# Optimization experiments

Measured on AMD Instinct MI355X. Metric: run time of the kernel, lower is better.

## Reference

```python
import jax, jax.numpy as jnp
import numpy as np

K = 5  # kernel_size per dim (dim=2 -> 25 kernels), B-spline degree 1, open spline


def spline_conv(x, edge_index, pseudo, W, root, bias):
    # x: [N, Cin], pseudo: [E, 2] in [0,1], W: [K*K, Cin, Cout]
    N = x.shape[0]
    src, dst = edge_index[0], edge_index[1]
    # Transform node features with every kernel weight once: [N, K*K, Cout]
    xk = jnp.einsum('ni,kio->nko', x, W)
    # Degree-1 open B-spline basis: v = u*(K-1); frac/1-frac weights over 2 knots per dim
    v = pseudo * (K - 1)
    bot = jnp.floor(v)
    frac = v - bot
    bot = bot.astype(jnp.int32)
    msg = jnp.zeros((src.shape[0], W.shape[2]), dtype=x.dtype)
    for s0 in (0, 1):
        for s1 in (0, 1):
            b0 = frac[:, 0] if s0 else (1.0 - frac[:, 0])
            b1 = frac[:, 1] if s1 else (1.0 - frac[:, 1])
            basis = b0 * b1  # [E]
            idx = (jnp.clip(bot[:, 0] + s0, 0, K - 1)
                   + K * jnp.clip(bot[:, 1] + s1, 0, K - 1))  # [E]
            msg = msg + basis[:, None] * xk[src, idx]  # gather [E, Cout]
    # scatter-max aggregation into target nodes; empty nodes -> 0 (PyG convention)
    agg = jax.ops.segment_max(msg, dst, num_segments=N)
    agg = jnp.where(jnp.isfinite(agg), agg, jnp.zeros_like(agg))
    return agg + x @ root + bias


def setup_inputs() -> dict:
    key = jax.random.key(0)
    ks = jax.random.split(key, 8)
    N, E, C = 50000, 1600000, 64
    Cin = C
    s = 1.0 / np.sqrt(25 * Cin)
    return {
        'x': jax.random.normal(ks[0], (N, C), dtype=jnp.float32),
        'edge_index': jax.random.randint(ks[1], (2, E), 0, N, dtype=jnp.int32),
        'edge_attr': jax.random.uniform(ks[2], (E, 2), dtype=jnp.float32),
        'W1': jax.random.normal(ks[3], (25, C, C), dtype=jnp.float32) * s,
        'root1': jax.random.normal(ks[4], (C, C), dtype=jnp.float32) / np.sqrt(C),
        'bias1': jnp.zeros((C,), dtype=jnp.float32),
        'W2': jax.random.normal(ks[5], (25, C, C), dtype=jnp.float32) * s,
        'root2': jax.random.normal(ks[6], (C, C), dtype=jnp.float32) / np.sqrt(C),
        'bias2': jnp.zeros((C,), dtype=jnp.float32),
    }


def reference(x, edge_index, edge_attr, W1, root1, bias1, W2, root2, bias2):
    h = jax.nn.relu(spline_conv(x, edge_index, edge_attr, W1, root1, bias1))
    out = spline_conv(h, edge_index, edge_attr, W2, root2, bias2)
    return out
```

## Files before the change

kernel.cpp:

```cpp
#include <hip/hip_runtime.h>
#include <hip/hip_bf16.h>
#include <math.h>

#define CHANNELS 64
#define KK 25
#define NBLK 26
#define NCOL (NBLK * CHANNELS)
#define NTILES (NCOL / 16)
#define ROWP 2560
#define CELL_BYTES 8192

#define BK_SHIFT 7
#define BK_W 128
#define BK_CAP 5120
#define BK_MAXNB 512
#define EDGES_PER_BLK 4096

typedef __attribute__((ext_vector_type(8))) short bf16x8;
typedef __attribute__((ext_vector_type(4))) float f32x4;
typedef __attribute__((ext_vector_type(2))) float f32x2;
typedef unsigned int u32;

__device__ __forceinline__ u32 f2bfu(float f) {
    u32 u = __float_as_uint(f);
    return (u + 0x7FFFu + ((u >> 16) & 1u)) >> 16;
}
__device__ __forceinline__ short f2bf(float f) { return (short)f2bfu(f); }

__device__ __forceinline__ void async_copy16(const void* g, void* l) {
    __builtin_amdgcn_global_load_lds(
        (const __attribute__((address_space(1))) u32*)g,
        (__attribute__((address_space(3))) u32*)l, 16, 0, 0);
}

template<int N> struct IC { static constexpr int v = N; };
template<int G, int GEND, class F>
__device__ __forceinline__ void unrollg(F f) {
    if constexpr (G < GEND) { f(IC<G>{}); unrollg<G + 1, GEND>(f); }
}

__device__ constexpr int cell_stores(int c) {
    return (c < KK) ? (((c % 5) != 0) ? 4 : 0) : 4;
}


__global__ __launch_bounds__(256) void prep_w(const float* __restrict__ W,
                                              const float* __restrict__ root,
                                              __hip_bfloat16* __restrict__ Wb) {
    int idx = blockIdx.x * 256 + threadIdx.x;
    if (idx >= NTILES * 2 * 64 * 8) return;
    int j = idx & 7;
    int l = (idx >> 3) & 63;
    int q = (idx >> 9) & 1;
    int t = idx >> 10;
    int cell = t >> 2;
    int o    = 4 * (l & 15) + (t & 3);
    int k    = q * 32 + (l >> 4) * 8 + j;
    float src = (cell < KK) ? W[cell * 4096 + k * 64 + o] : root[k * 64 + o];
    ((unsigned short*)Wb)[idx] = (unsigned short)f2bf(src);
}

__device__ __forceinline__ uint2 mkrec(int src, float v0f, float v1f) {
    const float v0 = v0f * 4.0f, v1 = v1f * 4.0f;
    const int p0 = max(min((int)floorf(v0), 3), 0);
    const int p1 = max(min((int)floorf(v1), 3), 0);
    const float f0 = v0 - (float)p0;
    const float f1 = v1 - (float)p1;
    const u32 f0q = min((u32)(f0 * 65536.0f), 65535u);
    const u32 f1q = min((u32)(f1 * 65536.0f), 65535u);
    uint2 rec;
    rec.x = (u32)src | ((u32)p0 << 16) | ((u32)p1 << 19);
    rec.y = f0q | (f1q << 16);
    return rec;
}


__global__ __launch_bounds__(256) void bucket_scatter(
    const int* __restrict__ ei, const float* __restrict__ ps,
    u32* __restrict__ bcur, uint2* __restrict__ bucketed, int E, int NB)
{
    __shared__ u32 lhist[BK_MAXNB];
    __shared__ u32 lbase[BK_MAXNB];
    const int t = threadIdx.x;
    const int e0 = blockIdx.x * EDGES_PER_BLK;
    for (int k = t; k < NB; k += 256) lhist[k] = 0;
    __syncthreads();
    u32 pk[16];
#pragma unroll
    for (int r = 0; r < 16; ++r) {
        const int e = e0 + r * 256 + t;
        u32 v = 0u;
        if (e < E) {
            const int bkt = ei[E + e] >> BK_SHIFT;
            const u32 lr = atomicAdd(&lhist[bkt], 1u);
            v = ((u32)bkt << 13) | lr;
        }
        pk[r] = v;
    }
    __syncthreads();
    for (int k = t; k < NB; k += 256) {
        const u32 h = lhist[k];
        lbase[k] = h ? atomicAdd(&bcur[k], h) : 0u;
    }
    __syncthreads();
#pragma unroll
    for (int r = 0; r < 16; ++r) {
        const int e = e0 + r * 256 + t;
        if (e < E) {
            const u32 v = pk[r];
            const int bkt = (int)(v >> 13);
            const u32 lr = v & 0x1FFFu;
            u32 slot = lbase[bkt] + lr;
            if (slot >= BK_CAP) slot = BK_CAP - 1;
            const int src = ei[e];
            const int dst = ei[E + e];
            uint2 rec = mkrec(src, ps[2 * e], ps[2 * e + 1]);
            rec.x |= (u32)(dst & (BK_W - 1)) << 22;
            bucketed[(size_t)bkt * BK_CAP + slot] = rec;
        }
    }
}

__global__ __launch_bounds__(256) void bucket_bases(
    const u32* __restrict__ bcur, u32* __restrict__ bbase, int NB)
{
    __shared__ u32 tmp[BK_MAXNB];
    const int t = threadIdx.x;
    for (int k = t; k < NB; k += 256) tmp[k] = min(bcur[k], (u32)BK_CAP);
    __syncthreads();
    if (t == 0) {
        u32 run = 0;
        for (int k = 0; k < NB; ++k) { const u32 c = tmp[k]; tmp[k] = run; run += c; }
    }
    __syncthreads();
    for (int k = t; k < NB; k += 256) bbase[k] = tmp[k];
}

__global__ __launch_bounds__(256) void bucket_sort(
    const uint2* __restrict__ bucketed, const u32* __restrict__ bcur,
    const u32* __restrict__ bbase, uint2* __restrict__ sorted,
    u32* __restrict__ cursor, int N)
{
    __shared__ __align__(16) uint2 buf[BK_CAP];
    __shared__ u32 lhist[BK_W + 1];
    __shared__ u32 lbase[BK_W + 1];
    const int b = blockIdx.x;
    const int t = threadIdx.x;
    const int cnt = (int)min(bcur[b], (u32)BK_CAP);
    const u32 gb = bbase[b];
    const uint2* __restrict__ in = bucketed + (size_t)b * BK_CAP;

    for (int k = t; k <= BK_W; k += 256) lhist[k] = 0;
    __syncthreads();
    for (int i = t; i < cnt; i += 256) {
        const u32 nl = (in[i].x >> 22) & (BK_W - 1);
        atomicAdd(&lhist[nl], 1u);
    }
    __syncthreads();
    if (t == 0) {
        u32 run = 0;
        for (int k = 0; k <= BK_W; ++k) { const u32 c = lhist[k]; lhist[k] = run; run += c; }
    }
    __syncthreads();
    for (int k = t; k <= BK_W; k += 256) lbase[k] = lhist[k];
    __syncthreads();
    for (int i = t; i < cnt; i += 256) {
        const uint2 r = in[i];
        const u32 nl = (r.x >> 22) & (BK_W - 1);
        const u32 p = atomicAdd(&lhist[nl], 1u);
        buf[p] = r;
    }
    __syncthreads();
    for (int i = t; i < cnt; i += 256) sorted[gb + i] = buf[i];
    for (int k = t; k <= BK_W; k += 256) {
        const int node = b * BK_W + k;
        if (node <= N) cursor[node] = gb + lbase[k];
    }
}

__global__ __launch_bounds__(256) void gemm_nb(
    const float* __restrict__ X, const __hip_bfloat16* __restrict__ Wb,
    char* __restrict__ XK, float* __restrict__ rootf, int N)
{
    __shared__ __align__(16) char lds[4][2][CELL_BYTES];
    const int lane = threadIdx.x & 63;
    const int wv   = threadIdx.x >> 6;
    const int rb   = blockIdx.x * 64 + wv * 16;
    const int m    = lane & 15;
    const int quad = lane >> 4;
    const int Nm1  = N - 1;

    const int rowc = min(rb + m, Nm1);
    const float* __restrict__ xp = X + (size_t)rowc * CHANNELS + quad * 8;
    float af[16];
    *(float4*)(af)      = *(const float4*)(xp);
    *(float4*)(af + 4)  = *(const float4*)(xp + 4);
    *(float4*)(af + 8)  = *(const float4*)(xp + 32);
    *(float4*)(af + 12) = *(const float4*)(xp + 36);
    bf16x8 A0, A1;
#pragma unroll
    for (int j = 0; j < 8; ++j) { A0[j] = f2bf(af[j]); A1[j] = f2bf(af[8 + j]); }

    const int r0 = rb + quad * 4;
    const char* __restrict__ wbc = (const char*)Wb;
    char* const ldsw = &lds[wv][0][0];

    auto stage = [&](int c, int buf) {
        const char* gsrc = wbc + (size_t)c * CELL_BYTES + lane * 16;
        char* lb = ldsw + buf * CELL_BYTES;
#pragma unroll
        for (int k = 0; k < 8; ++k)
            async_copy16(gsrc + k * 1024, lb + k * 1024);
    };

    u32 prevp[4] = {0u, 0u, 0u, 0u};

    stage(0, 0);
    stage(1, 1);

    unrollg<0, NBLK>([&](auto icc) {
        constexpr int c = decltype(icc)::v;
        constexpr int NC = (c == 0) ? 8
                         : cell_stores(c - 1) + ((c + 1 < NBLK) ? 8 : 0);
        asm volatile("s_waitcnt vmcnt(%0)" :: "i"(NC) : "memory");

        const char* cb = ldsw + (c & 1) * CELL_BYTES + lane * 16;
        f32x4 acc0 = {0.f, 0.f, 0.f, 0.f};
        f32x4 acc1 = {0.f, 0.f, 0.f, 0.f};
        f32x4 acc2 = {0.f, 0.f, 0.f, 0.f};
        f32x4 acc3 = {0.f, 0.f, 0.f, 0.f};
        acc0 = __builtin_amdgcn_mfma_f32_16x16x32_bf16(A0, *(const bf16x8*)(cb),        acc0, 0, 0, 0);
        acc0 = __builtin_amdgcn_mfma_f32_16x16x32_bf16(A1, *(const bf16x8*)(cb + 1024), acc0, 0, 0, 0);
        acc1 = __builtin_amdgcn_mfma_f32_16x16x32_bf16(A0, *(const bf16x8*)(cb + 2048), acc1, 0, 0, 0);
        acc1 = __builtin_amdgcn_mfma_f32_16x16x32_bf16(A1, *(const bf16x8*)(cb + 3072), acc1, 0, 0, 0);
        acc2 = __builtin_amdgcn_mfma_f32_16x16x32_bf16(A0, *(const bf16x8*)(cb + 4096), acc2, 0, 0, 0);
        acc2 = __builtin_amdgcn_mfma_f32_16x16x32_bf16(A1, *(const bf16x8*)(cb + 5120), acc2, 0, 0, 0);
        acc3 = __builtin_amdgcn_mfma_f32_16x16x32_bf16(A0, *(const bf16x8*)(cb + 6144), acc3, 0, 0, 0);
        acc3 = __builtin_amdgcn_mfma_f32_16x16x32_bf16(A1, *(const bf16x8*)(cb + 7168), acc3, 0, 0, 0);

        if constexpr (c < KK) {
            constexpr int d1 = c / 5;
            constexpr int d0 = c % 5;
            u32 pk[4];
#pragma unroll
            for (int i = 0; i < 4; ++i) {
                u32 p = __builtin_amdgcn_cvt_pk_fp8_f32(acc0[i], acc1[i], 0u, false);
                p = __builtin_amdgcn_cvt_pk_fp8_f32(acc2[i], acc3[i], p, true);
                pk[i] = p;
            }
            if constexpr (d0 >= 1) {
#pragma unroll
                for (int i = 0; i < 4; ++i) {
                    const int r = min(r0 + i, Nm1);
                    *(uint2*)(XK + (size_t)r * ROWP
                              + (d1 * 512 + (d0 - 1) * 128) + 8 * m) =
                        make_uint2(prevp[i], pk[i]);
                }
            }
#pragma unroll
            for (int i = 0; i < 4; ++i) prevp[i] = pk[i];
        } else {
#pragma unroll
            for (int i = 0; i < 4; ++i) {
                const int r = min(r0 + i, Nm1);
                *(float4*)(rootf + (size_t)r * CHANNELS + 4 * m) =
                    make_float4(acc0[i], acc1[i], acc2[i], acc3[i]);
            }
        }
        if constexpr (c + 2 < NBLK) {
            asm volatile("s_waitcnt lgkmcnt(0)" ::: "memory");
            stage(c + 2, c & 1);
        }
    });
}

__global__ __launch_bounds__(256) void agg_node_p(
    const uint2* __restrict__ sorted, const u32* __restrict__ cursor,
    const char* __restrict__ XK, const float* __restrict__ rootf,
    const float* __restrict__ bias, float* __restrict__ out, int N, int relu,
    int node_blocks, const float* __restrict__ Wsrc,
    const float* __restrict__ rootsrc, __hip_bfloat16* __restrict__ Wbdst)
{
    if ((int)blockIdx.x >= node_blocks) {
        int idx = ((int)blockIdx.x - node_blocks) * 256 + threadIdx.x;
        if (idx < NTILES * 2 * 64 * 8) {
            int j = idx & 7;
            int l = (idx >> 3) & 63;
            int q = (idx >> 9) & 1;
            int t = idx >> 10;
            int cell = t >> 2;
            int o    = 4 * (l & 15) + (t & 3);
            int k    = q * 32 + (l >> 4) * 8 + j;
            float s = (cell < KK) ? Wsrc[cell * 4096 + k * 64 + o] : rootsrc[k * 64 + o];
            ((unsigned short*)Wbdst)[idx] = (unsigned short)f2bf(s);
        }
        return;
    }
    const int lane = threadIdx.x & 63;
    const int n = blockIdx.x * 4 + (threadIdx.x >> 6);
    if (n >= N) return;
    const int q = lane >> 4, j = lane & 15;
    const int beg = (int)cursor[n];
    const int end = (int)cursor[n + 1];

    float m0 = -INFINITY, m1 = -INFINITY, m2 = -INFINITY, m3 = -INFINITY;
    if (beg < end) {
        const int last = end - 1;
#define GATHP(r, q0, q1)                                                       \
        {                                                                      \
            const char* b_ = XK + (size_t)((r).x & 0xffff) * ROWP + (j << 3);  \
            const int o_ = (((int)((r).x >> 16) & 7)                           \
                            + (((int)((r).x >> 19) & 7) << 2)) << 7;           \
            q0 = *(const uint2*)(b_ + o_);                                     \
            q1 = *(const uint2*)(b_ + o_ + 512);                               \
        }
        uint2 rA = sorted[min(beg + q,      last)];
        uint2 rB = sorted[min(beg + 4 + q,  last)];
        uint2 rC = sorted[min(beg + 8 + q,  last)];
        uint2 ga0, ga1, gb0, gb1, gc0, gc1;
        GATHP(rA, ga0, ga1)
        GATHP(rB, gb0, gb1)
        for (int i = beg; i < end; i += 4) {
            uint2 rD = sorted[min(i + 12 + q, last)];
            GATHP(rC, gc0, gc1)
            const float f0 = (float)(rA.y & 0xffff) * (1.0f / 65536.0f);
            const float f1 = (float)(rA.y >> 16)    * (1.0f / 65536.0f);
            const float w00 = (1.f - f0) * (1.f - f1);
            const float w10 = f0 * (1.f - f1);
            const float w01 = (1.f - f0) * f1;
            const float w11 = f0 * f1;
            f32x2 s01 = __builtin_amdgcn_cvt_pk_f32_fp8(ga0.x, false) * w00
                      + __builtin_amdgcn_cvt_pk_f32_fp8(ga0.y, false) * w10
                      + __builtin_amdgcn_cvt_pk_f32_fp8(ga1.x, false) * w01
                      + __builtin_amdgcn_cvt_pk_f32_fp8(ga1.y, false) * w11;
            f32x2 s23 = __builtin_amdgcn_cvt_pk_f32_fp8(ga0.x, true)  * w00
                      + __builtin_amdgcn_cvt_pk_f32_fp8(ga0.y, true)  * w10
                      + __builtin_amdgcn_cvt_pk_f32_fp8(ga1.x, true)  * w01
                      + __builtin_amdgcn_cvt_pk_f32_fp8(ga1.y, true)  * w11;
            m0 = fmaxf(m0, s01.x); m1 = fmaxf(m1, s01.y);
            m2 = fmaxf(m2, s23.x); m3 = fmaxf(m3, s23.y);
            rA = rB; rB = rC; rC = rD;
            ga0 = gb0; ga1 = gb1;
            gb0 = gc0; gb1 = gc1;
        }
#undef GATHP
    }
    m0 = fmaxf(m0, __shfl_xor(m0, 16, 64)); m0 = fmaxf(m0, __shfl_xor(m0, 32, 64));
    m1 = fmaxf(m1, __shfl_xor(m1, 16, 64)); m1 = fmaxf(m1, __shfl_xor(m1, 32, 64));
    m2 = fmaxf(m2, __shfl_xor(m2, 16, 64)); m2 = fmaxf(m2, __shfl_xor(m2, 32, 64));
    m3 = fmaxf(m3, __shfl_xor(m3, 16, 64)); m3 = fmaxf(m3, __shfl_xor(m3, 32, 64));
    const float a0 = isfinite(m0) ? m0 : 0.f;
    const float a1 = isfinite(m1) ? m1 : 0.f;
    const float a2 = isfinite(m2) ? m2 : 0.f;
    const float a3 = isfinite(m3) ? m3 : 0.f;

    const float4 rv = *(const float4*)(rootf + (size_t)n * CHANNELS + 4 * j);
    const float4 bv = *(const float4*)(bias + 4 * j);
    float r0 = a0 + rv.x + bv.x;
    float r1 = a1 + rv.y + bv.y;
    float r2 = a2 + rv.z + bv.z;
    float r3 = a3 + rv.w + bv.w;
    if (relu) {
        r0 = fmaxf(r0, 0.f); r1 = fmaxf(r1, 0.f);
        r2 = fmaxf(r2, 0.f); r3 = fmaxf(r3, 0.f);
    }
    if (q == 0)
        *(float4*)(out + (size_t)n * CHANNELS + 4 * j) = make_float4(r0, r1, r2, r3);
}

extern "C" void kernel_launch(void* const* d_in, const int* in_sizes, int n_in,
                              void* d_out, int out_size, void* d_ws, size_t ws_size,
                              hipStream_t stream) {
    const float* x     = (const float*)d_in[0];
    const int*   ei    = (const int*)d_in[1];
    const float* ps    = (const float*)d_in[2];
    const float* W1    = (const float*)d_in[3];
    const float* root1 = (const float*)d_in[4];
    const float* bias1 = (const float*)d_in[5];
    const float* W2    = (const float*)d_in[6];
    const float* root2 = (const float*)d_in[7];
    const float* bias2 = (const float*)d_in[8];
    float* out = (float*)d_out;

    const int N = in_sizes[0] / CHANNELS;
    const int E = in_sizes[1] / 2;
    const int NB = (N + BK_W - 1) / BK_W;

    char* ws = (char*)d_ws;
    char* xk = ws;
    size_t off = (size_t)N * ROWP;
    float* h = (float*)(ws + off);
    off += (size_t)N * CHANNELS * sizeof(float);
    float* rootf = (float*)(ws + off);
    off += (size_t)N * CHANNELS * sizeof(float);
    uint2* sorted = (uint2*)(ws + off);
    off += (size_t)E * sizeof(uint2);
    uint2* bucketed = (uint2*)(ws + off);
    off += (size_t)BK_MAXNB * BK_CAP * sizeof(uint2);
    u32* bcur = (u32*)(ws + off);
    off += (size_t)BK_MAXNB * 4;
    u32* bbase = (u32*)(ws + off);
    off += (size_t)BK_MAXNB * 4;
    __hip_bfloat16* Wb = (__hip_bfloat16*)(ws + off);
    off += (size_t)NTILES * 2 * 64 * 8 * 2;
    u32* cursor = (u32*)(ws + off);
    off += ((size_t)N + 1) * 4;

    const int prep_blocks = (NTILES * 2 * 64 * 8 + 255) / 256;
    const int gemm_blocks = (N + 63) / 64;
    const int node_blocks = (N + 3) / 4;
    const int bscat_blocks = (E + EDGES_PER_BLK - 1) / EDGES_PER_BLK;

    hipMemsetAsync(bcur, 0, (size_t)BK_MAXNB * 4, stream);
    prep_w<<<prep_blocks, 256, 0, stream>>>(W1, root1, Wb);

    bucket_scatter<<<bscat_blocks, 256, 0, stream>>>(ei, ps, bcur, bucketed, E, NB);
    bucket_bases<<<1, 256, 0, stream>>>(bcur, bbase, NB);
    bucket_sort<<<NB, 256, 0, stream>>>(bucketed, bcur, bbase, sorted, cursor, N);

    gemm_nb<<<gemm_blocks, 256, 0, stream>>>(x, Wb, xk, rootf, N);

    agg_node_p<<<node_blocks + prep_blocks, 256, 0, stream>>>(
        sorted, cursor, xk, rootf, bias1, h, N, 1, node_blocks, W2, root2, Wb);

    gemm_nb<<<gemm_blocks, 256, 0, stream>>>(h, Wb, xk, rootf, N);
    agg_node_p<<<node_blocks, 256, 0, stream>>>(
        sorted, cursor, xk, rootf, bias2, out, N, 0, node_blocks, W2, root2, Wb);
}
```

Before: 366.3 us.

## Stage GEMM weights in half-cells to halve LDS and deepen pipelining

The gemm_nb kernel now stages each 8KB weight cell as two 4KB halves, double-buffered. This halves the LDS per block from 64KB to 32KB so more blocks can be resident, and it interleaves loads with the MFMAs at a finer grain. The waitcnt accounting is reworked to match. Separately, bucket_scatter now loads src, dst and pseudo once in the first pass as a float2, and keeps the packed record in registers. This avoids re-reading them in the second pass, at the cost of more registers per thread.

After: 349.9 us. 4.5% less time.

```diff
diff --git a/kernel.cpp b/kernel.cpp
--- a/kernel.cpp
+++ b/kernel.cpp
@@ -8,7 +8,8 @@
 #define NCOL (NBLK * CHANNELS)
 #define NTILES (NCOL / 16)
 #define ROWP 2560
-#define CELL_BYTES 8192
+#define HALF_BYTES 4096
+#define NHALF (2 * NBLK)
 
 #define BK_SHIFT 7
 #define BK_W 128
@@ -85,17 +86,24 @@
     const int e0 = blockIdx.x * EDGES_PER_BLK;
     for (int k = t; k < NB; k += 256) lhist[k] = 0;
     __syncthreads();
-    u32 pk[16];
+    u32 meta[16];
+    uint2 recs[16];
 #pragma unroll
     for (int r = 0; r < 16; ++r) {
         const int e = e0 + r * 256 + t;
         u32 v = 0u;
+        uint2 rec = make_uint2(0u, 0u);
         if (e < E) {
-            const int bkt = ei[E + e] >> BK_SHIFT;
+            const int dst = ei[E + e];
+            const int bkt = dst >> BK_SHIFT;
             const u32 lr = atomicAdd(&lhist[bkt], 1u);
             v = ((u32)bkt << 13) | lr;
-        }
-        pk[r] = v;
+            const float2 pp = *(const float2*)(ps + 2 * e);
+            rec = mkrec(ei[e], pp.x, pp.y);
+            rec.x |= (u32)(dst & (BK_W - 1)) << 22;
+        }
+        meta[r] = v;
+        recs[r] = rec;
     }
     __syncthreads();
     for (int k = t; k < NB; k += 256) {
@@ -107,16 +115,10 @@
     for (int r = 0; r < 16; ++r) {
         const int e = e0 + r * 256 + t;
         if (e < E) {
-            const u32 v = pk[r];
-            const int bkt = (int)(v >> 13);
-            const u32 lr = v & 0x1FFFu;
-            u32 slot = lbase[bkt] + lr;
+            const int bkt = (int)(meta[r] >> 13);
+            u32 slot = lbase[bkt] + (meta[r] & 0x1FFFu);
             if (slot >= BK_CAP) slot = BK_CAP - 1;
-            const int src = ei[e];
-            const int dst = ei[E + e];
-            uint2 rec = mkrec(src, ps[2 * e], ps[2 * e + 1]);
-            rec.x |= (u32)(dst & (BK_W - 1)) << 22;
-            bucketed[(size_t)bkt * BK_CAP + slot] = rec;
+            bucketed[(size_t)bkt * BK_CAP + slot] = recs[r];
         }
     }
 }
@@ -182,7 +184,7 @@
     const float* __restrict__ X, const __hip_bfloat16* __restrict__ Wb,
     char* __restrict__ XK, float* __restrict__ rootf, int N)
 {
-    __shared__ __align__(16) char lds[4][2][CELL_BYTES];
+    __shared__ __align__(16) char lds[4][2][HALF_BYTES];
     const int lane = threadIdx.x & 63;
     const int wv   = threadIdx.x >> 6;
     const int rb   = blockIdx.x * 64 + wv * 16;
@@ -205,71 +207,78 @@
     const char* __restrict__ wbc = (const char*)Wb;
     char* const ldsw = &lds[wv][0][0];
 
-    auto stage = [&](int c, int buf) {
-        const char* gsrc = wbc + (size_t)c * CELL_BYTES + lane * 16;
-        char* lb = ldsw + buf * CELL_BYTES;
-#pragma unroll
-        for (int k = 0; k < 8; ++k)
+    auto stage = [&](int h, int buf) {
+        const char* gsrc = wbc + (size_t)h * HALF_BYTES + lane * 16;
+        char* lb = ldsw + buf * HALF_BYTES;
+#pragma unroll
+        for (int k = 0; k < 4; ++k)
             async_copy16(gsrc + k * 1024, lb + k * 1024);
     };
 
     u32 prevp[4] = {0u, 0u, 0u, 0u};
+    f32x4 acc0 = {0.f, 0.f, 0.f, 0.f};
+    f32x4 acc1 = {0.f, 0.f, 0.f, 0.f};
+    f32x4 acc2, acc3;
 
     stage(0, 0);
     stage(1, 1);
 
-    unrollg<0, NBLK>([&](auto icc) {
-        constexpr int c = decltype(icc)::v;
-        constexpr int NC = (c == 0) ? 8
-                         : cell_stores(c - 1) + ((c + 1 < NBLK) ? 8 : 0);
+    unrollg<0, NHALF>([&](auto ich) {
+        constexpr int h = decltype(ich)::v;
+        constexpr int NC = ((h + 1 < NHALF) ? 4 : 0)
+                         + ((h % 2 == 0 && h >= 2) ? cell_stores((h - 2) / 2) : 0);
         asm volatile("s_waitcnt vmcnt(%0)" :: "i"(NC) : "memory");
 
-        const char* cb = ldsw + (c & 1) * CELL_BYTES + lane * 16;
-        f32x4 acc0 = {0.f, 0.f, 0.f, 0.f};
-        f32x4 acc1 = {0.f, 0.f, 0.f, 0.f};
-        f32x4 acc2 = {0.f, 0.f, 0.f, 0.f};
-        f32x4 acc3 = {0.f, 0.f, 0.f, 0.f};
-        acc0 = __builtin_amdgcn_mfma_f32_16x16x32_bf16(A0, *(const bf16x8*)(cb),        acc0, 0, 0, 0);
-        acc0 = __builtin_amdgcn_mfma_f32_16x16x32_bf16(A1, *(const bf16x8*)(cb + 1024), acc0, 0, 0, 0);
-        acc1 = __builtin_amdgcn_mfma_f32_16x16x32_bf16(A0, *(const bf16x8*)(cb + 2048), acc1, 0, 0, 0);
-        acc1 = __builtin_amdgcn_mfma_f32_16x16x32_bf16(A1, *(const bf16x8*)(cb + 3072), acc1, 0, 0, 0);
-        acc2 = __builtin_amdgcn_mfma_f32_16x16x32_bf16(A0, *(const bf16x8*)(cb + 4096), acc2, 0, 0, 0);
-        acc2 = __builtin_amdgcn_mfma_f32_16x16x32_bf16(A1, *(const bf16x8*)(cb + 5120), acc2, 0, 0, 0);
-        acc3 = __builtin_amdgcn_mfma_f32_16x16x32_bf16(A0, *(const bf16x8*)(cb + 6144), acc3, 0, 0, 0);
-        acc3 = __builtin_amdgcn_mfma_f32_16x16x32_bf16(A1, *(const bf16x8*)(cb + 7168), acc3, 0, 0, 0);
-
-        if constexpr (c < KK) {
-            constexpr int d1 = c / 5;
-            constexpr int d0 = c % 5;
-            u32 pk[4];
-#pragma unroll
-            for (int i = 0; i < 4; ++i) {
-                u32 p = __builtin_amdgcn_cvt_pk_fp8_f32(acc0[i], acc1[i], 0u, false);
-                p = __builtin_amdgcn_cvt_pk_fp8_f32(acc2[i], acc3[i], p, true);
-                pk[i] = p;
-            }
-            if constexpr (d0 >= 1) {
+        const char* cb = ldsw + (h & 1) * HALF_BYTES + lane * 16;
+        if constexpr ((h & 1) == 0) {
+            acc0 = {0.f, 0.f, 0.f, 0.f};
+            acc1 = {0.f, 0.f, 0.f, 0.f};
+            acc0 = __builtin_amdgcn_mfma_f32_16x16x32_bf16(A0, *(const bf16x8*)(cb),        acc0, 0, 0, 0);
+            acc0 = __builtin_amdgcn_mfma_f32_16x16x32_bf16(A1, *(const bf16x8*)(cb + 1024), acc0, 0, 0, 0);
+            acc1 = __builtin_amdgcn_mfma_f32_16x16x32_bf16(A0, *(const bf16x8*)(cb + 2048), acc1, 0, 0, 0);
+            acc1 = __builtin_amdgcn_mfma_f32_16x16x32_bf16(A1, *(const bf16x8*)(cb + 3072), acc1, 0, 0, 0);
+        } else {
+            acc2 = {0.f, 0.f, 0.f, 0.f};
+            acc3 = {0.f, 0.f, 0.f, 0.f};
+            acc2 = __builtin_amdgcn_mfma_f32_16x16x32_bf16(A0, *(const bf16x8*)(cb),        acc2, 0, 0, 0);
+            acc2 = __builtin_amdgcn_mfma_f32_16x16x32_bf16(A1, *(const bf16x8*)(cb + 1024), acc2, 0, 0, 0);
+            acc3 = __builtin_amdgcn_mfma_f32_16x16x32_bf16(A0, *(const bf16x8*)(cb + 2048), acc3, 0, 0, 0);
+            acc3 = __builtin_amdgcn_mfma_f32_16x16x32_bf16(A1, *(const bf16x8*)(cb + 3072), acc3, 0, 0, 0);
+
+            constexpr int c = (h - 1) / 2;
+            if constexpr (c < KK) {
+                constexpr int d1 = c / 5;
+                constexpr int d0 = c % 5;
+                u32 pk[4];
+#pragma unroll
+                for (int i = 0; i < 4; ++i) {
+                    u32 p = __builtin_amdgcn_cvt_pk_fp8_f32(acc0[i], acc1[i], 0u, false);
+                    p = __builtin_amdgcn_cvt_pk_fp8_f32(acc2[i], acc3[i], p, true);
+                    pk[i] = p;
+                }
+                if constexpr (d0 >= 1) {
+#pragma unroll
+                    for (int i = 0; i < 4; ++i) {
+                        const int r = min(r0 + i, Nm1);
+                        *(uint2*)(XK + (size_t)r * ROWP
+                                  + (d1 * 512 + (d0 - 1) * 128) + 8 * m) =
+                            make_uint2(prevp[i], pk[i]);
+                    }
+                }
+#pragma unroll
+                for (int i = 0; i < 4; ++i) prevp[i] = pk[i];
+            } else {
 #pragma unroll
                 for (int i = 0; i < 4; ++i) {
                     const int r = min(r0 + i, Nm1);
-                    *(uint2*)(XK + (size_t)r * ROWP
-                              + (d1 * 512 + (d0 - 1) * 128) + 8 * m) =
-                        make_uint2(prevp[i], pk[i]);
+                    *(float4*)(rootf + (size_t)r * CHANNELS + 4 * m) =
+                        make_float4(acc0[i], acc1[i], acc2[i], acc3[i]);
                 }
             }
-#pragma unroll
-            for (int i = 0; i < 4; ++i) prevp[i] = pk[i];
-        } else {
-#pragma unroll
-            for (int i = 0; i < 4; ++i) {
-                const int r = min(r0 + i, Nm1);
-                *(float4*)(rootf + (size_t)r * CHANNELS + 4 * m) =
-                    make_float4(acc0[i], acc1[i], acc2[i], acc3[i]);
-            }
-        }
-        if constexpr (c + 2 < NBLK) {
+        }
+        if constexpr (h + 2 < NHALF) {
             asm volatile("s_waitcnt lgkmcnt(0)" ::: "memory");
-            stage(c + 2, c & 1);
+            stage(h + 2, h & 1);
         }
     });
 }
```
